# Optimization experiments

Hardware: AMD Instinct MI355X
Metric: run time of the kernel (lower is better)

The kernel has to match this reference:

```python
import jax, jax.numpy as jnp
import numpy as np

B, S, D, H = 2, 2048, 1024, 16
DK = D // H


def setup_inputs() -> dict:
    key = jax.random.key(0)
    ks = jax.random.split(key, 12)
    scale = 1.0 / np.sqrt(D)
    inp = {
        "query": jax.random.normal(ks[0], (B, S, D), jnp.float32),
        "key": jax.random.normal(ks[1], (B, S, D), jnp.float32),
        "value": jax.random.normal(ks[2], (B, S, D), jnp.float32),
        "mask": jnp.broadcast_to(jnp.tril(jnp.ones((S, S), bool)), (B, S, S)),
        "Wq": jax.random.normal(ks[3], (D, D), jnp.float32) * scale,
        "bq": jnp.zeros((D,), jnp.float32),
        "Wk": jax.random.normal(ks[4], (D, D), jnp.float32) * scale,
        "bk": jnp.zeros((D,), jnp.float32),
        "Wv": jax.random.normal(ks[5], (D, D), jnp.float32) * scale,
        "bv": jnp.zeros((D,), jnp.float32),
        "Wo": jax.random.normal(ks[6], (D, D), jnp.float32) * scale,
        "bo": jnp.zeros((D,), jnp.float32),
    }
    return inp


def _split_heads(x):
    # [B, S, D] -> [B, H, S, DK]
    return x.reshape(B, S, H, DK).transpose(0, 2, 1, 3)


def reference(query, key, value, mask, Wq, bq, Wk, bk, Wv, bv, Wo, bo):
    q = _split_heads(query @ Wq + bq)
    k = _split_heads(key @ Wk + bk)
    v = _split_heads(value @ Wv + bv)
    # scores: [B, H, S, S]
    scores = jnp.einsum("bhqd,bhkd->bhqk", q, k) / jnp.sqrt(jnp.float32(DK))
    scores = jnp.where(mask[:, None, :, :], scores, jnp.float32(-1e9))
    p_attn = jax.nn.softmax(scores, axis=-1)
    x = jnp.einsum("bhqk,bhkd->bhqd", p_attn, v)  # [B, H, S, DK]
    x = x.transpose(0, 2, 1, 3).reshape(B, S, D)
    return x @ Wo + bo
```

## Files before the change

### kernel.cpp

```cpp
#include <hip/hip_runtime.h>


#define S_LEN 2048
#define DMODEL 1024
#define NHEAD 16
#define DKH 64
#define QSCALE 0.18033688011112042f

typedef __attribute__((ext_vector_type(8))) short short8;
typedef __attribute__((ext_vector_type(4))) float f32x4;
typedef __attribute__((ext_vector_type(4))) unsigned short ushort4v;

__device__ __forceinline__ unsigned short f2bf(float f) {
  union { float f; unsigned int u; } v; v.f = f;
  unsigned int r = v.u + 0x7fffu + ((v.u >> 16) & 1u);
  return (unsigned short)(r >> 16);
}

__device__ __forceinline__ unsigned int cvtpk_bf16(float lo, float hi) {
  unsigned int d;
  asm("v_cvt_pk_bf16_f32 %0, %1, %2" : "=v"(d) : "v"(lo), "v"(hi));
  return d;
}

__device__ __forceinline__ void gload_lds16(const void* g, void* l) {
  __builtin_amdgcn_global_load_lds(
      (const __attribute__((address_space(1))) void*)g,
      (__attribute__((address_space(3))) void*)l, 16, 0, 0);
}

__global__ __launch_bounds__(256) void transpose_cast4(
    const float* __restrict__ W0, const float* __restrict__ W1,
    const float* __restrict__ W2, const float* __restrict__ W3,
    unsigned short* __restrict__ T0, unsigned short* __restrict__ T1,
    unsigned short* __restrict__ T2, unsigned short* __restrict__ T3) {
  __shared__ float tile[32][33];
  const int z = blockIdx.z;
  const float* W = (z == 0) ? W0 : (z == 1) ? W1 : (z == 2) ? W2 : W3;
  unsigned short* Wt = (z == 0) ? T0 : (z == 1) ? T1 : (z == 2) ? T2 : T3;
  const int tx = threadIdx.x, ty = threadIdx.y;
  const int c0 = blockIdx.x * 32, r0 = blockIdx.y * 32;
#pragma unroll
  for (int i = 0; i < 32; i += 8)
    tile[ty + i][tx] = W[(r0 + ty + i) * 1024 + c0 + tx];
  __syncthreads();
#pragma unroll
  for (int i = 0; i < 32; i += 8)
    Wt[(c0 + ty + i) * 1024 + r0 + tx] = f2bf(tile[tx][ty + i]);
}

__global__ __launch_bounds__(256) void cast3(const float* __restrict__ s0,
                                             const float* __restrict__ s1,
                                             const float* __restrict__ s2,
                                             unsigned short* __restrict__ d0,
                                             unsigned short* __restrict__ d1,
                                             unsigned short* __restrict__ d2) {
  const int z = blockIdx.y;
  const float* src = (z == 0) ? s0 : (z == 1) ? s1 : s2;
  unsigned short* dst = (z == 0) ? d0 : (z == 1) ? d1 : d2;
  const int i = (blockIdx.x * 256 + threadIdx.x) * 8;
  float4 a = *(const float4*)&src[i];
  float4 b = *(const float4*)&src[i + 4];
  unsigned short u[8];
  u[0] = f2bf(a.x); u[1] = f2bf(a.y); u[2] = f2bf(a.z); u[3] = f2bf(a.w);
  u[4] = f2bf(b.x); u[5] = f2bf(b.y); u[6] = f2bf(b.z); u[7] = f2bf(b.w);
  *(short8*)&dst[i] = *(short8*)u;
}

__global__ __launch_bounds__(256) void qkv_gemm(
    const unsigned short* Qc, const unsigned short* Kc, const unsigned short* Vc,
    const unsigned short* WtQ, const unsigned short* WtK, const unsigned short* WtV,
    const float* bq, const float* bk, const float* bv,
    unsigned short* Qw, unsigned short* Kw, unsigned short* Vtw) {
  __shared__ unsigned short Alds[2][4096];
  __shared__ unsigned short Blds[2][4096];
  const int z = blockIdx.z;
  const unsigned short* A  = (z == 0) ? Qc : (z == 1) ? Kc : Vc;
  const unsigned short* Wt = (z == 0) ? WtQ : (z == 1) ? WtK : WtV;
  const float* bias        = (z == 0) ? bq : (z == 1) ? bk : bv;

  const int tid = threadIdx.x;
  const int m0 = blockIdx.x * 128, n0 = blockIdx.y * 128;
  const int wid = tid >> 6, lane = tid & 63;
  const int lg = lane >> 4, lr = lane & 15;
  const int wr = (wid >> 1) * 64, wc = (wid & 1) * 64;
  const int srow_base = wid * 32 + (lane >> 2);
  const int scol = (lane & 3) * 8;

  f32x4 acc[4][4] = {};

#define GSTAGE(BUF, KT)                                                          \
  {                                                                              \
    _Pragma("unroll")                                                            \
    for (int i = 0; i < 2; i++) {                                                \
      const int row = srow_base + i * 16;                                        \
      gload_lds16(A  + (m0 + row) * 1024 + (KT) + scol,                          \
                  (char*)&Alds[BUF][0] + wid * 2048 + i * 1024);                 \
      gload_lds16(Wt + (n0 + row) * 1024 + (KT) + scol,                          \
                  (char*)&Blds[BUF][0] + wid * 2048 + i * 1024);                 \
    }                                                                            \
  }

  GSTAGE(0, 0)
  int cur = 0;
  for (int kt = 0; kt < 1024; kt += 32) {
    __syncthreads();
    if (kt + 32 < 1024) GSTAGE(cur ^ 1, kt + 32)
    short8 af[4], bfr[4];
#pragma unroll
    for (int i = 0; i < 4; i++) af[i] = *(short8*)&Alds[cur][(wr + i * 16 + lr) * 32 + lg * 8];
#pragma unroll
    for (int i = 0; i < 4; i++) bfr[i] = *(short8*)&Blds[cur][(wc + i * 16 + lr) * 32 + lg * 8];
#pragma unroll
    for (int mi = 0; mi < 4; mi++)
#pragma unroll
      for (int ni = 0; ni < 4; ni++)
        acc[mi][ni] = __builtin_amdgcn_mfma_f32_16x16x32_bf16(af[mi], bfr[ni], acc[mi][ni], 0, 0, 0);
    cur ^= 1;
  }
#undef GSTAGE

  if (z < 2) {
    unsigned short* O = (z == 0) ? Qw : Kw;
    const float sc = (z == 0) ? QSCALE : 1.0f;
#pragma unroll
    for (int mi = 0; mi < 4; mi++)
#pragma unroll
      for (int ni = 0; ni < 4; ni++) {
        const int gn = n0 + wc + ni * 16 + lr;
        const int h = gn >> 6, dk = gn & 63;
        const float bb = bias[gn];
#pragma unroll
        for (int r = 0; r < 4; r++) {
          const int gm = m0 + wr + mi * 16 + lg * 4 + r;
          const int b = gm >> 11, s = gm & 2047;
          O[(((b * NHEAD + h) * S_LEN + s) << 6) + dk] = f2bf((acc[mi][ni][r] + bb) * sc);
        }
      }
  } else {
#pragma unroll
    for (int mi = 0; mi < 4; mi++)
#pragma unroll
      for (int ni = 0; ni < 4; ni++) {
        const int gn = n0 + wc + ni * 16 + lr;
        const int h = gn >> 6, dk = gn & 63;
        const float bb = bias[gn];
        const int gm = m0 + wr + mi * 16 + lg * 4;
        const int b = gm >> 11, s = gm & 2047;
        const int s6 = s & 63;
        const int np = (s & ~63) + ((s6 >> 5) << 5) + (((s6 >> 2) & 3) << 3) +
                       (((s6 >> 4) & 1) << 2);
        unsigned short u[4];
#pragma unroll
        for (int r = 0; r < 4; r++) u[r] = f2bf(acc[mi][ni][r] + bb);
        *(ushort4v*)&Vtw[(((b * NHEAD + h) * DKH + dk) << 11) + np] = *(ushort4v*)u;
      }
  }
}

__global__ __launch_bounds__(256) void oproj_gemm(const unsigned short* __restrict__ A,
                                                  const unsigned short* __restrict__ Wt,
                                                  const float* __restrict__ bias,
                                                  float* __restrict__ Of32) {
  __shared__ unsigned short Alds[2][2048];
  __shared__ unsigned short Blds[2][4096];
  const int tid = threadIdx.x;
  const int m0 = blockIdx.x * 64, n0 = blockIdx.y * 128;
  const int wid = tid >> 6, lane = tid & 63;
  const int lg = lane >> 4, lr = lane & 15;
  const int wc = wid * 32;
  const int arow = wid * 16 + (lane >> 2);
  const int brow_base = wid * 32 + (lane >> 2);
  const int scol = (lane & 3) * 8;

  f32x4 acc[4][2] = {};

#define OSTAGE(BUF, KT)                                                          \
  {                                                                              \
    gload_lds16(A + (m0 + arow) * 1024 + (KT) + scol,                            \
                (char*)&Alds[BUF][0] + wid * 1024);                              \
    _Pragma("unroll")                                                            \
    for (int i = 0; i < 2; i++) {                                                \
      const int row = brow_base + i * 16;                                        \
      gload_lds16(Wt + (n0 + row) * 1024 + (KT) + scol,                          \
                  (char*)&Blds[BUF][0] + wid * 2048 + i * 1024);                 \
    }                                                                            \
  }

  OSTAGE(0, 0)
  int cur = 0;
  for (int kt = 0; kt < 1024; kt += 32) {
    __syncthreads();
    if (kt + 32 < 1024) OSTAGE(cur ^ 1, kt + 32)
    short8 af[4], bfr[2];
#pragma unroll
    for (int i = 0; i < 4; i++) af[i] = *(short8*)&Alds[cur][(i * 16 + lr) * 32 + lg * 8];
#pragma unroll
    for (int j = 0; j < 2; j++) bfr[j] = *(short8*)&Blds[cur][(wc + j * 16 + lr) * 32 + lg * 8];
#pragma unroll
    for (int mi = 0; mi < 4; mi++)
#pragma unroll
      for (int ni = 0; ni < 2; ni++)
        acc[mi][ni] = __builtin_amdgcn_mfma_f32_16x16x32_bf16(af[mi], bfr[ni], acc[mi][ni], 0, 0, 0);
    cur ^= 1;
  }
#undef OSTAGE

#pragma unroll
  for (int mi = 0; mi < 4; mi++)
#pragma unroll
    for (int ni = 0; ni < 2; ni++) {
      const int gn = n0 + wc + ni * 16 + lr;
      const float bb = bias[gn];
#pragma unroll
      for (int r = 0; r < 4; r++) {
        const int gm = m0 + mi * 16 + lg * 4 + r;
        Of32[gm * 1024 + gn] = acc[mi][ni][r] + bb;
      }
    }
}

__global__ __launch_bounds__(256) void attn_k(const unsigned short* __restrict__ Q,
                                              const unsigned short* __restrict__ K,
                                              const unsigned short* __restrict__ Vt,
                                              unsigned short* __restrict__ X) {
  __shared__ unsigned short Kb[2][4096];
  __shared__ unsigned short Vb[2][4096];
  const int tid = threadIdx.x;
  const int wid = tid >> 6, lane = tid & 63;
  const int lg = lane >> 4, lr = lane & 15;
  const int bh = blockIdx.y;
  const unsigned short* Qh = Q + bh * (S_LEN * DKH);
  const char* KhB = (const char*)(K + bh * (S_LEN * DKH));
  const char* VtB = (const char*)(Vt + bh * (DKH * S_LEN));
  const int b = bh >> 4, h = bh & 15;

  const int srow_lo = (lane >> 3);
  const int scolb = (lane & 7) * 16;

  short8 ones8;
#pragma unroll
  for (int i = 0; i < 8; i++) ones8[i] = (short)0x3F80;

  const int qt = 31 - (int)blockIdx.x;
  const int qr = qt * 64 + wid * 16;

  short8 qf[2];
#pragma unroll
  for (int c = 0; c < 2; c++) qf[c] = *(const short8*)&Qh[(qr + lr) * 64 + c * 32 + lg * 8];

  f32x4 o[4] = {};
  f32x4 lsv = {};

  int cur = 0;

#define STAGE(BUF, KV)                                                          \
  {                                                                             \
    _Pragma("unroll")                                                           \
    for (int i = 0; i < 2; i++) {                                               \
      const int row = wid * 16 + i * 8 + srow_lo;                               \
      const int sw = scolb ^ ((row & 7) << 4);                                  \
      gload_lds16(KhB + ((KV) + row) * 128 + sw,                                \
                  (char*)&Kb[BUF][0] + wid * 2048 + i * 1024);                  \
      gload_lds16(VtB + row * 4096 + (KV) * 2 + sw,                             \
                  (char*)&Vb[BUF][0] + wid * 2048 + i * 1024);                  \
    }                                                                           \
  }

  STAGE(cur, 0);

  for (int t = 0; t <= qt; ++t) {
    __syncthreads();
    if (t < qt) STAGE(cur ^ 1, (t + 1) * 64);
    const bool diag = (t == qt);

    f32x4 sa[4] = {};
    __builtin_amdgcn_s_setprio(1);
#pragma unroll
    for (int jf = 0; jf < 4; jf++) {
      const int row = jf * 16 + lr;
#pragma unroll
      for (int c = 0; c < 2; c++) {
        const int cb = (c * 64 + lg * 16) ^ ((lr & 7) << 4);
        short8 kf = *(const short8*)((const char*)&Kb[cur][0] + row * 128 + cb);
        sa[jf] = __builtin_amdgcn_mfma_f32_16x16x32_bf16(kf, qf[c], sa[jf], 0, 0, 0);
      }
    }
    __builtin_amdgcn_s_setprio(0);

    float p[4][4];
    if (diag) {
      const int qloc = wid * 16 + lr;
#pragma unroll
      for (int jf = 0; jf < 4; jf++)
#pragma unroll
        for (int r = 0; r < 4; r++) {
          const float e = exp2f(sa[jf][r]);
          p[jf][r] = (jf * 16 + lg * 4 + r > qloc) ? 0.f : e;
        }
    } else {
#pragma unroll
      for (int jf = 0; jf < 4; jf++)
#pragma unroll
        for (int r = 0; r < 4; r++) p[jf][r] = exp2f(sa[jf][r]);
    }

    union { short8 v; unsigned int u[4]; } pk[2];
#pragma unroll
    for (int c = 0; c < 2; c++) {
      pk[c].u[0] = cvtpk_bf16(p[2 * c][0], p[2 * c][1]);
      pk[c].u[1] = cvtpk_bf16(p[2 * c][2], p[2 * c][3]);
      pk[c].u[2] = cvtpk_bf16(p[2 * c + 1][0], p[2 * c + 1][1]);
      pk[c].u[3] = cvtpk_bf16(p[2 * c + 1][2], p[2 * c + 1][3]);
    }

    __builtin_amdgcn_s_setprio(1);
#pragma unroll
    for (int f = 0; f < 4; f++) {
      const char* vrow = (const char*)&Vb[cur][0] + (f * 16 + lr) * 128;
      const int swz = (lr & 7) << 4;
#pragma unroll
      for (int c = 0; c < 2; c++) {
        short8 vf = *(const short8*)(vrow + ((c * 64 + lg * 16) ^ swz));
        o[f] = __builtin_amdgcn_mfma_f32_16x16x32_bf16(pk[c].v, vf, o[f], 0, 0, 0);
      }
    }
#pragma unroll
    for (int c = 0; c < 2; c++)
      lsv = __builtin_amdgcn_mfma_f32_16x16x32_bf16(pk[c].v, ones8, lsv, 0, 0, 0);
    __builtin_amdgcn_s_setprio(0);
    cur ^= 1;
  }

#pragma unroll
  for (int r = 0; r < 4; r++) {
    const float inv = 1.f / lsv[r];
    const int q = qr + lg * 4 + r;
#pragma unroll
    for (int f = 0; f < 4; f++)
      X[(b * S_LEN + q) * DMODEL + h * DKH + f * 16 + lr] = f2bf(o[f][r] * inv);
  }
#undef STAGE
}

extern "C" void kernel_launch(void* const* d_in, const int* in_sizes, int n_in,
                              void* d_out, int out_size, void* d_ws, size_t ws_size,
                              hipStream_t stream) {
  const float* query = (const float*)d_in[0];
  const float* key   = (const float*)d_in[1];
  const float* value = (const float*)d_in[2];
  const float* Wq = (const float*)d_in[4];
  const float* bq = (const float*)d_in[5];
  const float* Wk = (const float*)d_in[6];
  const float* bk = (const float*)d_in[7];
  const float* Wv = (const float*)d_in[8];
  const float* bv = (const float*)d_in[9];
  const float* Wo = (const float*)d_in[10];
  const float* bo = (const float*)d_in[11];
  float* out = (float*)d_out;

  unsigned short* ws = (unsigned short*)d_ws;
  unsigned short* WtQ = ws;
  unsigned short* WtK = ws + 1048576;
  unsigned short* WtV = ws + 2097152;
  unsigned short* WtO = ws + 3145728;
  unsigned short* Qw  = ws + 4194304;
  unsigned short* Kw  = ws + 8388608;
  unsigned short* Vtw = ws + 12582912;
  unsigned short* Xw  = ws + 16777216;
  unsigned short* Qc  = ws + 20971520;
  unsigned short* Kc  = ws + 25165824;
  unsigned short* Vc  = ws + 29360128;
  (void)in_sizes; (void)n_in; (void)out_size; (void)ws_size;

  transpose_cast4<<<dim3(32, 32, 4), dim3(32, 8), 0, stream>>>(
      Wq, Wk, Wv, Wo, WtQ, WtK, WtV, WtO);

  cast3<<<dim3(2048, 3), 256, 0, stream>>>(query, key, value, Qc, Kc, Vc);

  qkv_gemm<<<dim3(32, 8, 3), 256, 0, stream>>>(Qc, Kc, Vc, WtQ, WtK, WtV,
                                               bq, bk, bv, Qw, Kw, Vtw);

  attn_k<<<dim3(32, 32), 256, 0, stream>>>(Qw, Kw, Vtw, Xw);

  oproj_gemm<<<dim3(64, 8), 256, 0, stream>>>(Xw, WtO, bo, out);
}
```

Before: 146.0 us.

## Pair causal query tiles per block and give each wave two query fragments

The attention kernel now runs 2-wave blocks, and each wave handles 32 query rows, so every K/V fragment read from LDS feeds two MFMAs. Each block processes two query tiles in sequence (tile i and tile 31-i), which gives every block the same total causal work. The aim is better load balance across the grid and less LDS traffic per MFMA. In exchange it uses more registers per wave, launches fewer waves in total (512 blocks of 128 threads), and puts the two passes one after the other inside a block.

```diff
diff --git a/kernel.cpp b/kernel.cpp
--- a/kernel.cpp
+++ b/kernel.cpp
@@ -220,7 +220,7 @@
     }
 }
 
-__global__ __launch_bounds__(256) void attn_k(const unsigned short* __restrict__ Q,
+__global__ __launch_bounds__(128) void attn_k(const unsigned short* __restrict__ Q,
                                               const unsigned short* __restrict__ K,
                                               const unsigned short* __restrict__ Vt,
                                               unsigned short* __restrict__ X) {
@@ -242,103 +242,120 @@
 #pragma unroll
   for (int i = 0; i < 8; i++) ones8[i] = (short)0x3F80;
 
-  const int qt = 31 - (int)blockIdx.x;
-  const int qr = qt * 64 + wid * 16;
-
-  short8 qf[2];
-#pragma unroll
-  for (int c = 0; c < 2; c++) qf[c] = *(const short8*)&Qh[(qr + lr) * 64 + c * 32 + lg * 8];
-
-  f32x4 o[4] = {};
-  f32x4 lsv = {};
-
-  int cur = 0;
+  for (int pass = 0; pass < 2; ++pass) {
+    const int qt = (pass == 0) ? (int)blockIdx.x : 31 - (int)blockIdx.x;
+    const int qr = qt * 64 + wid * 32;
+
+    short8 qf[2][2];
+#pragma unroll
+    for (int qh = 0; qh < 2; qh++)
+#pragma unroll
+      for (int c = 0; c < 2; c++)
+        qf[qh][c] = *(const short8*)&Qh[(qr + qh * 16 + lr) * 64 + c * 32 + lg * 8];
+
+    f32x4 o[2][4] = {};
+    f32x4 lsv[2] = {};
+
+    int cur = 0;
+    __syncthreads();
 
 #define STAGE(BUF, KV)                                                          \
-  {                                                                             \
-    _Pragma("unroll")                                                           \
-    for (int i = 0; i < 2; i++) {                                               \
-      const int row = wid * 16 + i * 8 + srow_lo;                               \
-      const int sw = scolb ^ ((row & 7) << 4);                                  \
-      gload_lds16(KhB + ((KV) + row) * 128 + sw,                                \
-                  (char*)&Kb[BUF][0] + wid * 2048 + i * 1024);                  \
-      gload_lds16(VtB + row * 4096 + (KV) * 2 + sw,                             \
-                  (char*)&Vb[BUF][0] + wid * 2048 + i * 1024);                  \
-    }                                                                           \
-  }
-
-  STAGE(cur, 0);
-
-  for (int t = 0; t <= qt; ++t) {
-    __syncthreads();
-    if (t < qt) STAGE(cur ^ 1, (t + 1) * 64);
-    const bool diag = (t == qt);
-
-    f32x4 sa[4] = {};
-    __builtin_amdgcn_s_setprio(1);
-#pragma unroll
-    for (int jf = 0; jf < 4; jf++) {
-      const int row = jf * 16 + lr;
-#pragma unroll
-      for (int c = 0; c < 2; c++) {
-        const int cb = (c * 64 + lg * 16) ^ ((lr & 7) << 4);
-        short8 kf = *(const short8*)((const char*)&Kb[cur][0] + row * 128 + cb);
-        sa[jf] = __builtin_amdgcn_mfma_f32_16x16x32_bf16(kf, qf[c], sa[jf], 0, 0, 0);
-      }
+    {                                                                           \
+      _Pragma("unroll")                                                         \
+      for (int i = 0; i < 4; i++) {                                             \
+        const int row = wid * 32 + i * 8 + srow_lo;                             \
+        const int sw = scolb ^ ((row & 7) << 4);                                \
+        gload_lds16(KhB + ((KV) + row) * 128 + sw,                              \
+                    (char*)&Kb[BUF][0] + wid * 4096 + i * 1024);                \
+        gload_lds16(VtB + row * 4096 + (KV) * 2 + sw,                           \
+                    (char*)&Vb[BUF][0] + wid * 4096 + i * 1024);                \
+      }                                                                         \
     }
-    __builtin_amdgcn_s_setprio(0);
-
-    float p[4][4];
-    if (diag) {
-      const int qloc = wid * 16 + lr;
-#pragma unroll
-      for (int jf = 0; jf < 4; jf++)
-#pragma unroll
-        for (int r = 0; r < 4; r++) {
-          const float e = exp2f(sa[jf][r]);
-          p[jf][r] = (jf * 16 + lg * 4 + r > qloc) ? 0.f : e;
+
+    STAGE(cur, 0);
+
+    for (int t = 0; t <= qt; ++t) {
+      __syncthreads();
+      if (t < qt) STAGE(cur ^ 1, (t + 1) * 64);
+      const bool diag = (t == qt);
+
+      f32x4 sa[2][4] = {};
+      __builtin_amdgcn_s_setprio(1);
+#pragma unroll
+      for (int jf = 0; jf < 4; jf++) {
+        const int row = jf * 16 + lr;
+#pragma unroll
+        for (int c = 0; c < 2; c++) {
+          const int cb = (c * 64 + lg * 16) ^ ((lr & 7) << 4);
+          short8 kf = *(const short8*)((const char*)&Kb[cur][0] + row * 128 + cb);
+          sa[0][jf] = __builtin_amdgcn_mfma_f32_16x16x32_bf16(kf, qf[0][c], sa[0][jf], 0, 0, 0);
+          sa[1][jf] = __builtin_amdgcn_mfma_f32_16x16x32_bf16(kf, qf[1][c], sa[1][jf], 0, 0, 0);
         }
-    } else {
-#pragma unroll
-      for (int jf = 0; jf < 4; jf++)
-#pragma unroll
-        for (int r = 0; r < 4; r++) p[jf][r] = exp2f(sa[jf][r]);
+      }
+      __builtin_amdgcn_s_setprio(0);
+
+      float p[2][4][4];
+#pragma unroll
+      for (int qh = 0; qh < 2; qh++) {
+        if (diag) {
+          const int qloc = wid * 32 + qh * 16 + lr;
+#pragma unroll
+          for (int jf = 0; jf < 4; jf++)
+#pragma unroll
+            for (int r = 0; r < 4; r++) {
+              const float e = exp2f(sa[qh][jf][r]);
+              p[qh][jf][r] = (jf * 16 + lg * 4 + r > qloc) ? 0.f : e;
+            }
+        } else {
+#pragma unroll
+          for (int jf = 0; jf < 4; jf++)
+#pragma unroll
+            for (int r = 0; r < 4; r++) p[qh][jf][r] = exp2f(sa[qh][jf][r]);
+        }
+      }
+
+      union { short8 v; unsigned int u[4]; } pk[2][2];
+#pragma unroll
+      for (int qh = 0; qh < 2; qh++)
+#pragma unroll
+        for (int c = 0; c < 2; c++) {
+          pk[qh][c].u[0] = cvtpk_bf16(p[qh][2 * c][0], p[qh][2 * c][1]);
+          pk[qh][c].u[1] = cvtpk_bf16(p[qh][2 * c][2], p[qh][2 * c][3]);
+          pk[qh][c].u[2] = cvtpk_bf16(p[qh][2 * c + 1][0], p[qh][2 * c + 1][1]);
+          pk[qh][c].u[3] = cvtpk_bf16(p[qh][2 * c + 1][2], p[qh][2 * c + 1][3]);
+        }
+
+      __builtin_amdgcn_s_setprio(1);
+#pragma unroll
+      for (int f = 0; f < 4; f++) {
+        const char* vrow = (const char*)&Vb[cur][0] + (f * 16 + lr) * 128;
+        const int swz = (lr & 7) << 4;
+#pragma unroll
+        for (int c = 0; c < 2; c++) {
+          short8 vf = *(const short8*)(vrow + ((c * 64 + lg * 16) ^ swz));
+          o[0][f] = __builtin_amdgcn_mfma_f32_16x16x32_bf16(pk[0][c].v, vf, o[0][f], 0, 0, 0);
+          o[1][f] = __builtin_amdgcn_mfma_f32_16x16x32_bf16(pk[1][c].v, vf, o[1][f], 0, 0, 0);
+        }
+      }
+#pragma unroll
+      for (int qh = 0; qh < 2; qh++)
+#pragma unroll
+        for (int c = 0; c < 2; c++)
+          lsv[qh] = __builtin_amdgcn_mfma_f32_16x16x32_bf16(pk[qh][c].v, ones8, lsv[qh], 0, 0, 0);
+      __builtin_amdgcn_s_setprio(0);
+      cur ^= 1;
     }
 
-    union { short8 v; unsigned int u[4]; } pk[2];
-#pragma unroll
-    for (int c = 0; c < 2; c++) {
-      pk[c].u[0] = cvtpk_bf16(p[2 * c][0], p[2 * c][1]);
-      pk[c].u[1] = cvtpk_bf16(p[2 * c][2], p[2 * c][3]);
-      pk[c].u[2] = cvtpk_bf16(p[2 * c + 1][0], p[2 * c + 1][1]);
-      pk[c].u[3] = cvtpk_bf16(p[2 * c + 1][2], p[2 * c + 1][3]);
-    }
-
-    __builtin_amdgcn_s_setprio(1);
-#pragma unroll
-    for (int f = 0; f < 4; f++) {
-      const char* vrow = (const char*)&Vb[cur][0] + (f * 16 + lr) * 128;
-      const int swz = (lr & 7) << 4;
-#pragma unroll
-      for (int c = 0; c < 2; c++) {
-        short8 vf = *(const short8*)(vrow + ((c * 64 + lg * 16) ^ swz));
-        o[f] = __builtin_amdgcn_mfma_f32_16x16x32_bf16(pk[c].v, vf, o[f], 0, 0, 0);
-      }
-    }
-#pragma unroll
-    for (int c = 0; c < 2; c++)
-      lsv = __builtin_amdgcn_mfma_f32_16x16x32_bf16(pk[c].v, ones8, lsv, 0, 0, 0);
-    __builtin_amdgcn_s_setprio(0);
-    cur ^= 1;
-  }
-
-#pragma unroll
-  for (int r = 0; r < 4; r++) {
-    const float inv = 1.f / lsv[r];
-    const int q = qr + lg * 4 + r;
-#pragma unroll
-    for (int f = 0; f < 4; f++)
-      X[(b * S_LEN + q) * DMODEL + h * DKH + f * 16 + lr] = f2bf(o[f][r] * inv);
+#pragma unroll
+    for (int qh = 0; qh < 2; qh++)
+#pragma unroll
+      for (int r = 0; r < 4; r++) {
+        const float inv = 1.f / lsv[qh][r];
+        const int q = qr + qh * 16 + lg * 4 + r;
+#pragma unroll
+        for (int f = 0; f < 4; f++)
+          X[(b * S_LEN + q) * DMODEL + h * DKH + f * 16 + lr] = f2bf(o[qh][f][r] * inv);
+      }
   }
 #undef STAGE
 }
@@ -381,7 +398,7 @@
   qkv_gemm<<<dim3(32, 8, 3), 256, 0, stream>>>(Qc, Kc, Vc, WtQ, WtK, WtV,
                                                bq, bk, bv, Qw, Kw, Vtw);
 
-  attn_k<<<dim3(32, 32), 256, 0, stream>>>(Qw, Kw, Vtw, Xw);
+  attn_k<<<dim3(16, 32), 128, 0, stream>>>(Qw, Kw, Vtw, Xw);
 
   oproj_gemm<<<dim3(64, 8), 256, 0, stream>>>(Xw, WtO, bo, out);
 }
```

After: 149.0 us. 1.02x slower.

## Pair complementary causal query tiles per attention block for load balance and K/V reuse

Applied to the files above, without the earlier changes.

Each attention workgroup now handles two query tiles, qt and 31-qt, so every block does the same amount of causal work, and the grid is halved. The staged K/V tiles in LDS serve both query tiles, which cuts redundant K/V loads. In exchange, register pressure roughly doubles (two sets of accumulators and Q fragments), which may lower occupancy, and the grid of 512 blocks is smaller relative to the CU count.

```diff
diff --git a/kernel.cpp b/kernel.cpp
--- a/kernel.cpp
+++ b/kernel.cpp
@@ -242,15 +242,20 @@
 #pragma unroll
   for (int i = 0; i < 8; i++) ones8[i] = (short)0x3F80;
 
-  const int qt = 31 - (int)blockIdx.x;
-  const int qr = qt * 64 + wid * 16;
-
-  short8 qf[2];
-#pragma unroll
-  for (int c = 0; c < 2; c++) qf[c] = *(const short8*)&Qh[(qr + lr) * 64 + c * 32 + lg * 8];
-
-  f32x4 o[4] = {};
-  f32x4 lsv = {};
+  const int qtA = (int)blockIdx.x;
+  const int qtB = 31 - qtA;
+  const int qrA = qtA * 64 + wid * 16;
+  const int qrB = qtB * 64 + wid * 16;
+
+  short8 qfA[2], qfB[2];
+#pragma unroll
+  for (int c = 0; c < 2; c++) {
+    qfA[c] = *(const short8*)&Qh[(qrA + lr) * 64 + c * 32 + lg * 8];
+    qfB[c] = *(const short8*)&Qh[(qrB + lr) * 64 + c * 32 + lg * 8];
+  }
+
+  f32x4 oA[4] = {}, oB[4] = {};
+  f32x4 lsvA = {}, lsvB = {};
 
   int cur = 0;
 
@@ -269,12 +274,13 @@
 
   STAGE(cur, 0);
 
-  for (int t = 0; t <= qt; ++t) {
+  for (int t = 0; t <= qtB; ++t) {
     __syncthreads();
-    if (t < qt) STAGE(cur ^ 1, (t + 1) * 64);
-    const bool diag = (t == qt);
-
-    f32x4 sa[4] = {};
+    if (t < qtB) STAGE(cur ^ 1, (t + 1) * 64);
+    const bool doA = (t <= qtA);
+    const bool diagA = (t == qtA), diagB = (t == qtB);
+
+    f32x4 saA[4] = {}, saB[4] = {};
     __builtin_amdgcn_s_setprio(1);
 #pragma unroll
     for (int jf = 0; jf < 4; jf++) {
@@ -283,35 +289,63 @@
       for (int c = 0; c < 2; c++) {
         const int cb = (c * 64 + lg * 16) ^ ((lr & 7) << 4);
         short8 kf = *(const short8*)((const char*)&Kb[cur][0] + row * 128 + cb);
-        sa[jf] = __builtin_amdgcn_mfma_f32_16x16x32_bf16(kf, qf[c], sa[jf], 0, 0, 0);
+        saB[jf] = __builtin_amdgcn_mfma_f32_16x16x32_bf16(kf, qfB[c], saB[jf], 0, 0, 0);
+        if (doA)
+          saA[jf] = __builtin_amdgcn_mfma_f32_16x16x32_bf16(kf, qfA[c], saA[jf], 0, 0, 0);
       }
     }
     __builtin_amdgcn_s_setprio(0);
 
-    float p[4][4];
-    if (diag) {
-      const int qloc = wid * 16 + lr;
+    const int qloc = wid * 16 + lr;
+    float pA[4][4], pB[4][4];
+    if (diagB) {
 #pragma unroll
       for (int jf = 0; jf < 4; jf++)
 #pragma unroll
         for (int r = 0; r < 4; r++) {
-          const float e = exp2f(sa[jf][r]);
-          p[jf][r] = (jf * 16 + lg * 4 + r > qloc) ? 0.f : e;
+          const float e = exp2f(saB[jf][r]);
+          pB[jf][r] = (jf * 16 + lg * 4 + r > qloc) ? 0.f : e;
         }
     } else {
 #pragma unroll
       for (int jf = 0; jf < 4; jf++)
 #pragma unroll
-        for (int r = 0; r < 4; r++) p[jf][r] = exp2f(sa[jf][r]);
-    }
-
-    union { short8 v; unsigned int u[4]; } pk[2];
+        for (int r = 0; r < 4; r++) pB[jf][r] = exp2f(saB[jf][r]);
+    }
+    if (doA) {
+      if (diagA) {
+#pragma unroll
+        for (int jf = 0; jf < 4; jf++)
+#pragma unroll
+          for (int r = 0; r < 4; r++) {
+            const float e = exp2f(saA[jf][r]);
+            pA[jf][r] = (jf * 16 + lg * 4 + r > qloc) ? 0.f : e;
+          }
+      } else {
+#pragma unroll
+        for (int jf = 0; jf < 4; jf++)
+#pragma unroll
+          for (int r = 0; r < 4; r++) pA[jf][r] = exp2f(saA[jf][r]);
+      }
+    }
+
+    union u32x4_t { short8 v; unsigned int u[4]; };
+    u32x4_t pkA[2], pkB[2];
 #pragma unroll
     for (int c = 0; c < 2; c++) {
-      pk[c].u[0] = cvtpk_bf16(p[2 * c][0], p[2 * c][1]);
-      pk[c].u[1] = cvtpk_bf16(p[2 * c][2], p[2 * c][3]);
-      pk[c].u[2] = cvtpk_bf16(p[2 * c + 1][0], p[2 * c + 1][1]);
-      pk[c].u[3] = cvtpk_bf16(p[2 * c + 1][2], p[2 * c + 1][3]);
+      pkB[c].u[0] = cvtpk_bf16(pB[2 * c][0], pB[2 * c][1]);
+      pkB[c].u[1] = cvtpk_bf16(pB[2 * c][2], pB[2 * c][3]);
+      pkB[c].u[2] = cvtpk_bf16(pB[2 * c + 1][0], pB[2 * c + 1][1]);
+      pkB[c].u[3] = cvtpk_bf16(pB[2 * c + 1][2], pB[2 * c + 1][3]);
+    }
+    if (doA) {
+#pragma unroll
+      for (int c = 0; c < 2; c++) {
+        pkA[c].u[0] = cvtpk_bf16(pA[2 * c][0], pA[2 * c][1]);
+        pkA[c].u[1] = cvtpk_bf16(pA[2 * c][2], pA[2 * c][3]);
+        pkA[c].u[2] = cvtpk_bf16(pA[2 * c + 1][0], pA[2 * c + 1][1]);
+        pkA[c].u[3] = cvtpk_bf16(pA[2 * c + 1][2], pA[2 * c + 1][3]);
+      }
     }
 
     __builtin_amdgcn_s_setprio(1);
@@ -322,23 +356,32 @@
 #pragma unroll
       for (int c = 0; c < 2; c++) {
         short8 vf = *(const short8*)(vrow + ((c * 64 + lg * 16) ^ swz));
-        o[f] = __builtin_amdgcn_mfma_f32_16x16x32_bf16(pk[c].v, vf, o[f], 0, 0, 0);
-      }
-    }
-#pragma unroll
-    for (int c = 0; c < 2; c++)
-      lsv = __builtin_amdgcn_mfma_f32_16x16x32_bf16(pk[c].v, ones8, lsv, 0, 0, 0);
+        oB[f] = __builtin_amdgcn_mfma_f32_16x16x32_bf16(pkB[c].v, vf, oB[f], 0, 0, 0);
+        if (doA)
+          oA[f] = __builtin_amdgcn_mfma_f32_16x16x32_bf16(pkA[c].v, vf, oA[f], 0, 0, 0);
+      }
+    }
+#pragma unroll
+    for (int c = 0; c < 2; c++) {
+      lsvB = __builtin_amdgcn_mfma_f32_16x16x32_bf16(pkB[c].v, ones8, lsvB, 0, 0, 0);
+      if (doA)
+        lsvA = __builtin_amdgcn_mfma_f32_16x16x32_bf16(pkA[c].v, ones8, lsvA, 0, 0, 0);
+    }
     __builtin_amdgcn_s_setprio(0);
     cur ^= 1;
   }
 
 #pragma unroll
   for (int r = 0; r < 4; r++) {
-    const float inv = 1.f / lsv[r];
-    const int q = qr + lg * 4 + r;
-#pragma unroll
-    for (int f = 0; f < 4; f++)
-      X[(b * S_LEN + q) * DMODEL + h * DKH + f * 16 + lr] = f2bf(o[f][r] * inv);
+    const float invA = 1.f / lsvA[r];
+    const float invB = 1.f / lsvB[r];
+    const int qA = qrA + lg * 4 + r;
+    const int qB = qrB + lg * 4 + r;
+#pragma unroll
+    for (int f = 0; f < 4; f++) {
+      X[(b * S_LEN + qA) * DMODEL + h * DKH + f * 16 + lr] = f2bf(oA[f][r] * invA);
+      X[(b * S_LEN + qB) * DMODEL + h * DKH + f * 16 + lr] = f2bf(oB[f][r] * invB);
+    }
   }
 #undef STAGE
 }
@@ -381,7 +424,7 @@
   qkv_gemm<<<dim3(32, 8, 3), 256, 0, stream>>>(Qc, Kc, Vc, WtQ, WtK, WtV,
                                                bq, bk, bv, Qw, Kw, Vtw);
 
-  attn_k<<<dim3(32, 32), 256, 0, stream>>>(Qw, Kw, Vtw, Xw);
+  attn_k<<<dim3(16, 32), 256, 0, stream>>>(Qw, Kw, Vtw, Xw);
 
   oproj_gemm<<<dim3(64, 8), 256, 0, stream>>>(Xw, WtO, bo, out);
 }
```

After: 142.4 us. -2.5%, faster.
